# Kernel optimization log

Hardware: AMD Instinct MI355X
Metric: run time of the kernel (lower is better)

## Reference

```python
import jax, jax.numpy as jnp
import numpy as np

EPS = 1e-5  # torch BatchNorm2d default


def _conv(x, w, padding):
    return jax.lax.conv_general_dilated(
        x, w, window_strides=(1, 1),
        padding=[(padding, padding), (padding, padding)],
        dimension_numbers=("NCHW", "OIHW", "NCHW"))


def _bn(x, gamma, beta):
    # training-mode batchnorm (biased variance), matching nn.BatchNorm2d forward
    mu = x.mean(axis=(0, 2, 3), keepdims=True)
    var = x.var(axis=(0, 2, 3), keepdims=True)
    xn = (x - mu) * jax.lax.rsqrt(var + EPS)
    return gamma[None, :, None, None] * xn + beta[None, :, None, None]


def _ste(x):
    # forward: sign(x); backward: pass gradient where |x| <= 1 (STE)
    m = (jnp.abs(x) <= 1.0).astype(x.dtype)
    s = jax.lax.stop_gradient(jnp.sign(x))
    return s + m * x - jax.lax.stop_gradient(m * x)


def _binconv(x, w, alpha, padding=1):
    # XNOR-style: sign both operands, full-precision conv, scale by alpha
    return _conv(jnp.sign(x), jnp.sign(w), padding) * alpha


def _maxpool2(x):
    return jax.lax.reduce_window(x, -jnp.inf, jax.lax.max,
                                 (1, 1, 2, 2), (1, 1, 2, 2), "VALID")


def setup_inputs() -> dict:
    key = jax.random.key(0)
    ks = jax.random.split(key, 8)

    def kaiming(k, shape):
        fan_out = shape[0] * shape[2] * shape[3]
        std = np.sqrt(2.0 / fan_out)
        return jax.random.normal(k, shape, dtype=jnp.float32) * std

    return {
        "x": jax.random.normal(ks[0], (128, 1, 128, 128), dtype=jnp.float32),
        # first conv (full precision) 1->32, k=3, pad=1
        "w1": kaiming(ks[1], (32, 1, 3, 3)),
        "b1": jnp.zeros((32,), jnp.float32),
        "g1": jnp.ones((32,), jnp.float32),
        "beta1": jnp.zeros((32,), jnp.float32),
        # BinaryConv2d 32->32
        "w2": kaiming(ks[2], (32, 32, 3, 3)),
        "a2": jnp.ones((1,), jnp.float32),
        "g2": jnp.ones((32,), jnp.float32),
        "beta2": jnp.zeros((32,), jnp.float32),
        # BinaryConv2d 32->64
        "w3": kaiming(ks[3], (64, 32, 3, 3)),
        "a3": jnp.ones((1,), jnp.float32),
        "g3": jnp.ones((64,), jnp.float32),
        "beta3": jnp.zeros((64,), jnp.float32),
        # BinaryConv2d 64->128
        "w4": kaiming(ks[4], (128, 64, 3, 3)),
        "a4": jnp.ones((1,), jnp.float32),
        # classifier 128->10
        "wf": jax.random.normal(ks[5], (10, 128), dtype=jnp.float32) * (1.0 / np.sqrt(128.0)),
        "bf": jnp.zeros((10,), jnp.float32),
    }


def reference(x, w1, b1, g1, beta1, w2, a2, g2, beta2, w3, a3, g3, beta3, w4, a4, wf, bf):
    h = _conv(x, w1, padding=1) + b1[None, :, None, None]   # [N,32,128,128]
    h = _bn(h, g1, beta1)
    h = _ste(h)
    h = _binconv(h, w2, a2)                                 # [N,32,128,128]
    h = _maxpool2(h)                                        # [N,32,64,64]
    h = _bn(h, g2, beta2)
    h = _ste(h)
    h = _binconv(h, w3, a3)                                 # [N,64,64,64]
    h = _maxpool2(h)                                        # [N,64,32,32]
    h = _bn(h, g3, beta3)
    h = _ste(h)
    h = _binconv(h, w4, a4)                                 # [N,128,32,32]
    h = h.mean(axis=(2, 3))                                 # AdaptiveAvgPool2d(1) -> [N,128]
    return h @ wf.T + bf                                    # [N,10]
```

## Files before the change

kernel.cpp:

```cpp
#include <hip/hip_runtime.h>
#include <stdint.h>

constexpr int NB = 128;

__global__ void pack_weights_all_kernel(const float* __restrict__ w2, const float* __restrict__ w3,
                                        const float* __restrict__ w4,
                                        uint32_t* __restrict__ wp2, uint32_t* __restrict__ wp3,
                                        uint32_t* __restrict__ wp4)
{
    int idx = blockIdx.x * blockDim.x + threadIdx.x;
    const float* w; uint32_t* o; int ICW, i;
    if (idx < 288)       { w = w2; o = wp2; ICW = 1; i = idx; }
    else if (idx < 864)  { w = w3; o = wp3; ICW = 1; i = idx - 288; }
    else if (idx < 3168) { w = w4; o = wp4; ICW = 2; i = idx - 864; }
    else return;
    int iw = i % ICW;
    int t  = (i / ICW) % 9;
    int oc = i / (9 * ICW);
    int IC = ICW * 32;
    uint32_t word = 0;
    for (int b = 0; b < 32; ++b) {
        float wv = w[(size_t)(oc * IC + (iw * 32 + b)) * 9 + t];
        word |= (wv > 0.f ? 1u : 0u) << b;
    }
    o[i] = word;
}

__global__ void zero4_kernel(uint4* __restrict__ p, int n4)
{
    int i = blockIdx.x * blockDim.x + threadIdx.x;
    int stride = gridDim.x * blockDim.x;
    uint4 z = {0u, 0u, 0u, 0u};
    for (; i < n4; i += stride) p[i] = z;
}

__device__ __forceinline__ void conv1_load9(const float* __restrict__ x, int p, float* xv)
{
    int n = p >> 14;
    int y = (p >> 7) & 127;
    int c = p & 127;
    const float* xn = x + (size_t)n * 16384;
    #pragma unroll
    for (int ky = 0; ky < 3; ++ky)
    #pragma unroll
    for (int kx = 0; kx < 3; ++kx) {
        int yy = y + ky - 1, cc = c + kx - 1;
        float v = 0.f;
        if (yy >= 0 && yy < 128 && cc >= 0 && cc < 128) v = xn[yy * 128 + cc];
        xv[ky * 3 + kx] = v;
    }
}

__global__ __launch_bounds__(256) void xcorr_kernel(const float* __restrict__ x,
                                                    float* __restrict__ partials)
{
    __shared__ float wbuf[4][64];
    int tid = threadIdx.x;
    float s[9], c[45];
    #pragma unroll
    for (int t = 0; t < 9; ++t) s[t] = 0.f;
    #pragma unroll
    for (int q = 0; q < 45; ++q) c[q] = 0.f;

    int base = blockIdx.x * 256 + tid;
    #pragma unroll 4
    for (int k = 0; k < 16; ++k) {
        float xv[9];
        conv1_load9(x, base + k * 131072, xv);
        #pragma unroll
        for (int t = 0; t < 9; ++t) {
            s[t] += xv[t];
            #pragma unroll
            for (int u = t; u < 9; ++u) {
                int q = t * (19 - t) / 2 + (u - t);
                c[q] = fmaf(xv[t], xv[u], c[q]);
            }
        }
    }
    #pragma unroll
    for (int t = 0; t < 9; ++t) {
        float a = s[t];
        #pragma unroll
        for (int off = 32; off >= 1; off >>= 1) a += __shfl_xor(a, off, 64);
        s[t] = a;
    }
    #pragma unroll
    for (int q = 0; q < 45; ++q) {
        float a = c[q];
        #pragma unroll
        for (int off = 32; off >= 1; off >>= 1) a += __shfl_xor(a, off, 64);
        c[q] = a;
    }
    int lane = tid & 63, wv = tid >> 6;
    if (lane == 0) {
        #pragma unroll
        for (int t = 0; t < 9; ++t) wbuf[wv][t] = s[t];
        #pragma unroll
        for (int q = 0; q < 45; ++q) wbuf[wv][9 + q] = c[q];
    }
    __syncthreads();
    if (tid < 54)
        partials[blockIdx.x * 64 + tid] =
            (wbuf[0][tid] + wbuf[1][tid]) + (wbuf[2][tid] + wbuf[3][tid]);
}

__global__ void compute_ss1_kernel(const double* __restrict__ dsums,
                                   const float* __restrict__ w1, const float* __restrict__ b1,
                                   const float* __restrict__ g1, const float* __restrict__ be1,
                                   float* __restrict__ ss)
{
    __shared__ double S[9], C[45];
    int tid = threadIdx.x;
    if (tid < 9) S[tid] = dsums[tid];
    else if (tid < 54) C[tid - 9] = dsums[tid];
    __syncthreads();
    if (tid >= 32) return;
    double b = (double)b1[tid];
    double w[9];
    #pragma unroll
    for (int t = 0; t < 9; ++t) w[t] = (double)w1[tid * 9 + t];
    double Sdot = 0.0, Q = 0.0;
    #pragma unroll
    for (int t = 0; t < 9; ++t) {
        Sdot += w[t] * S[t];
        #pragma unroll
        for (int u = t; u < 9; ++u) {
            int q = t * (19 - t) / 2 + (u - t);
            double term = w[t] * w[u] * C[q];
            Q += (u == t) ? term : 2.0 * term;
        }
    }
    const double N = 2097152.0;
    double mu  = Sdot / N + b;
    double ex2 = (Q + 2.0 * b * Sdot) / N + b * b;
    float var = (float)(ex2 - mu * mu);
    float A = g1[tid] * (1.f / sqrtf(var + 1e-5f));
    ss[tid] = A;
    ss[32 + tid] = be1[tid] - (float)mu * A;
}

template<int CH, int STRIDE>
__global__ __launch_bounds__(256) void reduce_partials_kernel(
    const float* __restrict__ partials, int nblk, double* __restrict__ dsums)
{
    __shared__ double wsum[4];
    int ch = blockIdx.x;
    int tid = threadIdx.x;
    double a = 0.0;
    for (int i = tid; i < nblk; i += 256)
        a += (double)partials[(size_t)i * STRIDE + ch];
    #pragma unroll
    for (int off = 32; off >= 1; off >>= 1)
        a += __shfl_xor(a, off, 64);
    if ((tid & 63) == 0) wsum[tid >> 6] = a;
    __syncthreads();
    if (tid == 0)
        dsums[ch] = (wsum[0] + wsum[1]) + (wsum[2] + wsum[3]);
}

__global__ __launch_bounds__(256) void conv1_pack2_kernel(
    const float* __restrict__ x, const float* __restrict__ w1, const float* __restrict__ b1,
    const float* __restrict__ ss, uint32_t* __restrict__ s1p)
{
    int p = blockIdx.x * 256 + threadIdx.x;
    float xv[9];
    conv1_load9(x, p, xv);
    int n = p >> 14, y = (p >> 7) & 127, c = p & 127;

    uint32_t word = 0;
    for (int oc = 0; oc < 32; ++oc) {
        float a = xv[0] * w1[oc * 9];
        #pragma unroll
        for (int t = 1; t < 9; ++t) a = fmaf(xv[t], w1[oc * 9 + t], a);
        float A = ss[oc];
        float Bc = fmaf(A, b1[oc], ss[32 + oc]);
        float v = fmaf(A, a, Bc);
        word |= (v > 0.f ? 1u : 0u) << oc;
    }
    s1p[(size_t)n * 16900 + (y + 1) * 130 + (c + 1)] = word;
}

template<int OC, int PW, int LPW, int MAINB>
__global__ __launch_bounds__(256) void binconv_mainfix_kernel(
    const uint32_t* __restrict__ sp_in, const uint32_t* __restrict__ wp,
    const float* __restrict__ alpha, uint32_t* __restrict__ m16)
{
    constexpr int PS = 2 * PW + 2;
    constexpr int TOTAL = NB * PW * PW;
    int tid = threadIdx.x;
    bool useMax = (alpha[0] >= 0.f);

    if ((int)blockIdx.x < MAINB) {
        int p = blockIdx.x * 256 + tid;
        int px = p & (PW - 1), py = (p >> LPW) & (PW - 1), n = p >> (2 * LPW);
        bool border = (px == 0) | (px == PW - 1) | (py == 0) | (py == PW - 1);
        const uint32_t* base = sp_in + (size_t)n * PS * PS + (2 * py) * PS + 2 * px;

        uint32_t xw[16];
        #pragma unroll
        for (int r = 0; r < 4; ++r) {
            uint2 a = *(const uint2*)(base + r * PS);
            uint2 b = *(const uint2*)(base + r * PS + 2);
            xw[r * 4 + 0] = a.x; xw[r * 4 + 1] = a.y;
            xw[r * 4 + 2] = b.x; xw[r * 4 + 3] = b.y;
        }

        uint32_t pend = 0;
        for (int oc = 0; oc < OC; ++oc) {
            int s0 = 0, s1 = 0, s2 = 0, s3 = 0;
            #pragma unroll
            for (int ky = 0; ky < 3; ++ky)
            #pragma unroll
            for (int kx = 0; kx < 3; ++kx) {
                uint32_t wt = wp[oc * 9 + ky * 3 + kx];
                s0 += __popc(xw[ky * 4 + kx]           ^ wt);
                s1 += __popc(xw[ky * 4 + kx + 1]       ^ wt);
                s2 += __popc(xw[(ky + 1) * 4 + kx]     ^ wt);
                s3 += __popc(xw[(ky + 1) * 4 + kx + 1] ^ wt);
            }
            int sm = useMax ? min(min(s0, s1), min(s2, s3))
                            : max(max(s0, s1), max(s2, s3));
            int m = 288 - 2 * sm;
            if ((oc & 1) == 0) pend = (uint32_t)(uint16_t)(short)m;
            else if (!border)
                m16[(size_t)(oc >> 1) * TOTAL + p] = pend | ((uint32_t)(uint16_t)(short)m << 16);
        }
    } else {
        constexpr int RING = 4 * PW - 4;
        int t = ((int)blockIdx.x - MAINB) * 256 + tid;
        if (t >= NB * RING) return;
        int n = t / RING, r = t % RING;
        int py, px;
        if (r < PW)              { py = 0;      px = r; }
        else if (r < 2 * PW)     { py = PW - 1; px = r - PW; }
        else if (r < 3 * PW - 2) { px = 0;      py = r - 2 * PW + 1; }
        else                     { px = PW - 1; py = r - (3 * PW - 2) + 1; }
        int p = n * PW * PW + py * PW + px;
        const uint32_t* base = sp_in + (size_t)n * PS * PS + (2 * py) * PS + 2 * px;

        uint32_t xw[16], wm[16];
        #pragma unroll
        for (int a = 0; a < 4; ++a) {
            int rr = 2 * py - 1 + a;
            bool rv = (rr >= 0) && (rr < 2 * PW);
            #pragma unroll
            for (int b = 0; b < 4; ++b) {
                int cc = 2 * px - 1 + b;
                bool v = rv && (cc >= 0) && (cc < 2 * PW);
                wm[a * 4 + b] = v ? 0xFFFFFFFFu : 0u;
                xw[a * 4 + b] = base[a * PS + b];
            }
        }
        int cnt[4];
        #pragma unroll
        for (int a2 = 0; a2 < 2; ++a2)
        #pragma unroll
        for (int b2 = 0; b2 < 2; ++b2) {
            int cc = 0;
            #pragma unroll
            for (int ky = 0; ky < 3; ++ky)
            #pragma unroll
            for (int kx = 0; kx < 3; ++kx)
                cc += (int)(wm[(a2 + ky) * 4 + (b2 + kx)] & 1u);
            cnt[a2 * 2 + b2] = cc * 32;
        }

        uint32_t pend = 0;
        for (int oc = 0; oc < OC; ++oc) {
            int v[4];
            #pragma unroll
            for (int a2 = 0; a2 < 2; ++a2)
            #pragma unroll
            for (int b2 = 0; b2 < 2; ++b2) {
                int pop = 0;
                #pragma unroll
                for (int ky = 0; ky < 3; ++ky)
                #pragma unroll
                for (int kx = 0; kx < 3; ++kx) {
                    int idx = (a2 + ky) * 4 + (b2 + kx);
                    pop += __popc((xw[idx] ^ wp[oc * 9 + ky * 3 + kx]) & wm[idx]);
                }
                v[a2 * 2 + b2] = cnt[a2 * 2 + b2] - 2 * pop;
            }
            int m = useMax ? max(max(v[0], v[1]), max(v[2], v[3]))
                           : min(min(v[0], v[1]), min(v[2], v[3]));
            if ((oc & 1) == 0) pend = (uint32_t)(uint16_t)(short)m;
            else m16[(size_t)(oc >> 1) * TOTAL + p] = pend | ((uint32_t)(uint16_t)(short)m << 16);
        }
    }
}

template<int PIXELS, int CHUNKS>
__global__ __launch_bounds__(256) void stats16_kernel(const uint32_t* __restrict__ m16,
                                                      double* __restrict__ pd)
{
    __shared__ int wb[4][4];
    int bid = blockIdx.x;
    int q = bid / CHUNKS, ch = bid % CHUNKS;
    const uint32_t* pl = m16 + (size_t)q * PIXELS + (size_t)ch * (PIXELS / CHUNKS);
    int tid = threadIdx.x;
    int s0 = 0, s1 = 0, q0 = 0, q1 = 0;
    #pragma unroll 4
    for (int j = 0; j < PIXELS / CHUNKS / 256; ++j) {
        uint32_t u = pl[tid + j * 256];
        int m0 = (int)(short)(u & 0xffffu);
        int m1 = (int)u >> 16;
        s0 += m0; s1 += m1;
        q0 += m0 * m0; q1 += m1 * m1;
    }
    #pragma unroll
    for (int off = 32; off >= 1; off >>= 1) {
        s0 += __shfl_xor(s0, off, 64); s1 += __shfl_xor(s1, off, 64);
        q0 += __shfl_xor(q0, off, 64); q1 += __shfl_xor(q1, off, 64);
    }
    int lane = tid & 63, w = tid >> 6;
    if (lane == 0) { wb[w][0] = s0; wb[w][1] = s1; wb[w][2] = q0; wb[w][3] = q1; }
    __syncthreads();
    if (tid < 4)
        pd[(size_t)bid * 4 + tid] =
            (double)((long long)wb[0][tid] + wb[1][tid] + wb[2][tid] + wb[3][tid]);
}

template<int OC, int CHUNKS>
__global__ void finalize16_kernel(const double* __restrict__ pd,
                                  const float* __restrict__ gamma, const float* __restrict__ beta,
                                  const float* __restrict__ alpha,
                                  float inv_n, float* __restrict__ ss)
{
    __shared__ double sums[2 * OC];
    int tid = threadIdx.x;
    if (tid < 2 * OC) {
        bool issq = tid >= OC;
        int c = issq ? tid - OC : tid;
        int q = c >> 1;
        int slot = (issq ? 2 : 0) + (c & 1);
        double a = 0.0;
        #pragma unroll 4
        for (int i = 0; i < CHUNKS; ++i)
            a += pd[(size_t)(q * CHUNKS + i) * 4 + slot];
        sums[tid] = a;
    }
    __syncthreads();
    if (tid < OC) {
        double al = (double)alpha[0];
        float mu  = (float)(sums[tid] * al * (double)inv_n);
        float ex2 = (float)(sums[OC + tid] * al * al * (double)inv_n);
        float var = ex2 - mu * mu;
        float A = gamma[tid] * (1.f / sqrtf(var + 1e-5f));
        ss[tid] = A;
        ss[OC + tid] = beta[tid] - mu * A;
    }
}

template<int OC, int PW, int LPW, bool PADOUT>
__global__ __launch_bounds__(256) void binconv_pack_kernel(
    const uint32_t* __restrict__ m16, const float* __restrict__ alpha,
    const float* __restrict__ ss, void* __restrict__ sout)
{
    constexpr int TOTAL = NB * PW * PW;
    __shared__ float Ap[OC], Bp[OC];
    int tid = threadIdx.x;
    if (tid < OC) { Ap[tid] = ss[tid] * alpha[0]; Bp[tid] = ss[OC + tid]; }
    __syncthreads();
    int p = blockIdx.x * 256 + tid;
    uint64_t word = 0;
    #pragma unroll
    for (int q = 0; q < OC / 2; ++q) {
        uint32_t u = m16[(size_t)q * TOTAL + p];
        int m0 = (int)(short)(u & 0xffffu);
        int m1 = (int)u >> 16;
        float v0 = fmaf(Ap[2 * q],     (float)m0, Bp[2 * q]);
        float v1 = fmaf(Ap[2 * q + 1], (float)m1, Bp[2 * q + 1]);
        word |= (v0 > 0.f ? 1ull : 0ull) << (2 * q);
        word |= (v1 > 0.f ? 1ull : 0ull) << (2 * q + 1);
    }
    if constexpr (PADOUT) {
        int px = p & (PW - 1), py = (p >> LPW) & (PW - 1), n = p >> (2 * LPW);
        ((uint32_t*)sout)[(size_t)n * (PW + 2) * (PW + 2) + (py + 1) * (PW + 2) + (px + 1)]
            = (uint32_t)word;
    } else {
        ((uint64_t*)sout)[p] = word;
    }
}

__global__ __launch_bounds__(256) void conv4_partial_kernel(
    const uint64_t* __restrict__ s3, const uint64_t* __restrict__ wp4,
    float* __restrict__ p4)
{
    __shared__ uint64_t xt[192];
    __shared__ uint64_t wl[1152];
    __shared__ float red[256];
    int b = blockIdx.x;
    int n = b >> 3, s = b & 7;
    int tid = threadIdx.x;
    for (int i = tid; i < 192; i += 256) {
        int row = 4 * s - 1 + (i >> 5);
        int col = i & 31;
        xt[i] = (row >= 0 && row < 32) ? s3[(size_t)n * 1024 + row * 32 + col] : 0ull;
    }
    for (int i = tid; i < 1152; i += 256) wl[i] = wp4[i];
    __syncthreads();
    int oc = tid & 127, h = tid >> 7;
    uint64_t wr[9];
    #pragma unroll
    for (int t = 0; t < 9; ++t) wr[t] = wl[oc * 9 + t];
    int acc = 0;
    #pragma unroll
    for (int ry = 0; ry < 2; ++ry) {
        int lry = 2 * h + ry;
        int y = 4 * s + lry;
        for (int x = 0; x < 32; ++x) {
            int pop = 0, c = 0;
            #pragma unroll
            for (int ky = 0; ky < 3; ++ky) {
                int yy = y + ky - 1;
                if (yy < 0 || yy >= 32) continue;
                int lrow = lry + ky;
                #pragma unroll
                for (int kx = 0; kx < 3; ++kx) {
                    int xx = x + kx - 1;
                    if (xx < 0 || xx >= 32) continue;
                    pop += __popcll(xt[lrow * 32 + xx] ^ wr[ky * 3 + kx]);
                    c += 64;
                }
            }
            acc += c - 2 * pop;
        }
    }
    red[tid] = (float)acc;
    __syncthreads();
    if (tid < 128)
        p4[(size_t)b * 128 + tid] = red[tid] + red[tid + 128];
}

__global__ __launch_bounds__(128) void mean_linear_kernel(
    const float* __restrict__ p4, const float* __restrict__ alpha4,
    const float* __restrict__ wf, const float* __restrict__ bf, float* __restrict__ out)
{
    __shared__ float ml[128];
    int n = blockIdx.x, tid = threadIdx.x;
    float a = 0.f;
    #pragma unroll
    for (int s = 0; s < 8; ++s)
        a += p4[(size_t)((n * 8 + s) * 128) + tid];
    ml[tid] = a * alpha4[0] * (1.f / 1024.f);
    __syncthreads();
    if (tid < 10) {
        const float* w = wf + tid * 128;
        float acc = bf[tid];
        #pragma unroll 4
        for (int i = 0; i < 128; ++i) acc = fmaf(ml[i], w[i], acc);
        out[n * 10 + tid] = acc;
    }
}

extern "C" void kernel_launch(void* const* d_in, const int* in_sizes, int n_in,
                              void* d_out, int out_size, void* d_ws, size_t ws_size,
                              hipStream_t stream)
{
    const float* x   = (const float*)d_in[0];
    const float* w1  = (const float*)d_in[1];
    const float* b1  = (const float*)d_in[2];
    const float* g1  = (const float*)d_in[3];
    const float* be1 = (const float*)d_in[4];
    const float* w2  = (const float*)d_in[5];
    const float* a2  = (const float*)d_in[6];
    const float* g2  = (const float*)d_in[7];
    const float* be2 = (const float*)d_in[8];
    const float* w3  = (const float*)d_in[9];
    const float* a3  = (const float*)d_in[10];
    const float* g3  = (const float*)d_in[11];
    const float* be3 = (const float*)d_in[12];
    const float* w4  = (const float*)d_in[13];
    const float* a4  = (const float*)d_in[14];
    const float* wf  = (const float*)d_in[15];
    const float* bf  = (const float*)d_in[16];
    float* out = (float*)d_out;

    uint8_t* ws = (uint8_t*)d_ws;
    size_t off = 0;
    auto alloc = [&](size_t bytes) -> void* {
        void* p = ws + off;
        off += (bytes + 255) & ~(size_t)255;
        return p;
    };
    uint32_t* wp2 = (uint32_t*)alloc(288 * 4);
    uint32_t* wp3 = (uint32_t*)alloc(576 * 4);
    uint32_t* wp4 = (uint32_t*)alloc(2304 * 4);
    float* ss1 = (float*)alloc(64 * 4);
    float* ss2 = (float*)alloc(64 * 4);
    float* ss3 = (float*)alloc(128 * 4);
    double* dsums = (double*)alloc(256 * 8);
    double* pd    = (double*)alloc(2048 * 8);
    float* partials = (float*)alloc((size_t)512 * 64 * 4);
    uint32_t* s1p = (uint32_t*)alloc((size_t)128 * 16900 * 4);
    uint32_t* s2p = (uint32_t*)alloc((size_t)128 * 4356 * 4);
    uint64_t* s3  = (uint64_t*)alloc((size_t)128 * 1024 * 8);
    float* p4    = (float*)alloc((size_t)1024 * 128 * 4);
    uint32_t* m16_2 = (uint32_t*)alloc((size_t)16 * 524288 * 4);
    uint32_t* m16_3 = (uint32_t*)alloc((size_t)32 * 131072 * 4);

    {
        size_t span_bytes = (size_t)((uint8_t*)(s2p + (size_t)128 * 4356) - (uint8_t*)s1p);
        int n4 = (int)(span_bytes / 16);
        zero4_kernel<<<1024, 256, 0, stream>>>((uint4*)s1p, n4);
    }

    pack_weights_all_kernel<<<13, 256, 0, stream>>>(w2, w3, w4, wp2, wp3, wp4);

    xcorr_kernel<<<512, 256, 0, stream>>>(x, partials);
    reduce_partials_kernel<54, 64><<<54, 256, 0, stream>>>(partials, 512, dsums);
    compute_ss1_kernel<<<1, 64, 0, stream>>>(dsums, w1, b1, g1, be1, ss1);
    conv1_pack2_kernel<<<8192, 256, 0, stream>>>(x, w1, b1, ss1, s1p);

    binconv_mainfix_kernel<32, 64, 6, 2048><<<2048 + 126, 256, 0, stream>>>(s1p, wp2, a2, m16_2);
    stats16_kernel<524288, 32><<<512, 256, 0, stream>>>(m16_2, pd);
    finalize16_kernel<32, 32><<<1, 256, 0, stream>>>(pd, g2, be2, a2, 1.f / 524288.f, ss2);
    binconv_pack_kernel<32, 64, 6, true><<<2048, 256, 0, stream>>>(m16_2, a2, ss2, (void*)s2p);

    binconv_mainfix_kernel<64, 32, 5, 512><<<512 + 62, 256, 0, stream>>>(s2p, wp3, a3, m16_3);
    stats16_kernel<131072, 8><<<256, 256, 0, stream>>>(m16_3, pd);
    finalize16_kernel<64, 8><<<1, 256, 0, stream>>>(pd, g3, be3, a3, 1.f / 131072.f, ss3);
    binconv_pack_kernel<64, 32, 5, false><<<512, 256, 0, stream>>>(m16_3, a3, ss3, (void*)s3);

    conv4_partial_kernel<<<1024, 256, 0, stream>>>(s3, (const uint64_t*)wp4, p4);
    mean_linear_kernel<<<128, 128, 0, stream>>>(p4, a4, wf, bf, out);
}
```

Measured before the change: 222.0 us.

## Quad-tile binconv, fuse stats finalize, zero only borders, merge ss1 reduction

Several changes at once. Only the padding borders are zeroed instead of the whole buffers. The partial reduction is merged with the ss1 computation, and the conv1 weights are prefolded with the BN scale and shift. The binary conv now computes a 2x2 block of pooled outputs per thread, with weights staged in LDS, so inputs are reused across neighbouring outputs. The stats finalize step is folded into the stats kernel using a last-block atomic counter. Together these aim to cut launch count and redundant memory traffic, at the cost of higher register pressure and fewer blocks in the conv kernels.

After: 298.6 us. 34.5% more time.

```diff
diff --git a/kernel.cpp b/kernel.cpp
--- a/kernel.cpp
+++ b/kernel.cpp
@@ -26,12 +26,30 @@
     o[i] = word;
 }
 
-__global__ void zero4_kernel(uint4* __restrict__ p, int n4)
-{
-    int i = blockIdx.x * blockDim.x + threadIdx.x;
-    int stride = gridDim.x * blockDim.x;
-    uint4 z = {0u, 0u, 0u, 0u};
-    for (; i < n4; i += stride) p[i] = z;
+__global__ void zero_borders_kernel(uint32_t* __restrict__ s1p, uint32_t* __restrict__ s2p,
+                                    uint32_t* __restrict__ counters)
+{
+    int t = blockIdx.x * 256 + threadIdx.x;
+    if (t < 4) counters[t] = 0u;
+    const int total1 = 128 * 516;
+    if (t < total1) {
+        int n = t / 516, i = t % 516;
+        int r, c;
+        if (i < 130)      { r = 0;   c = i; }
+        else if (i < 260) { r = 129; c = i - 130; }
+        else { int j = i - 260; r = 1 + (j >> 1); c = (j & 1) ? 129 : 0; }
+        s1p[(size_t)n * 16900 + r * 130 + c] = 0u;
+    }
+    int t2 = t - total1;
+    const int total2 = 128 * 260;
+    if (t2 >= 0 && t2 < total2) {
+        int n = t2 / 260, i = t2 % 260;
+        int r, c;
+        if (i < 66)       { r = 0;  c = i; }
+        else if (i < 132) { r = 65; c = i - 66; }
+        else { int j = i - 132; r = 1 + (j >> 1); c = (j & 1) ? 65 : 0; }
+        s2p[(size_t)n * 4356 + r * 66 + c] = 0u;
+    }
 }
 
 __device__ __forceinline__ void conv1_load9(const float* __restrict__ x, int p, float* xv)
@@ -104,15 +122,35 @@
             (wbuf[0][tid] + wbuf[1][tid]) + (wbuf[2][tid] + wbuf[3][tid]);
 }
 
-__global__ void compute_ss1_kernel(const double* __restrict__ dsums,
-                                   const float* __restrict__ w1, const float* __restrict__ b1,
-                                   const float* __restrict__ g1, const float* __restrict__ be1,
-                                   float* __restrict__ ss)
-{
+__global__ __launch_bounds__(512) void reduce_ss1_kernel(
+    const float* __restrict__ partials, const float* __restrict__ w1, const float* __restrict__ b1,
+    const float* __restrict__ g1, const float* __restrict__ be1,
+    float* __restrict__ ss, float* __restrict__ w1f)
+{
+    __shared__ double red[54][8];
     __shared__ double S[9], C[45];
     int tid = threadIdx.x;
-    if (tid < 9) S[tid] = dsums[tid];
-    else if (tid < 54) C[tid - 9] = dsums[tid];
+    int ch = tid >> 3, part = tid & 7;
+    if (ch < 54) {
+        double a0 = 0.0, a1 = 0.0, a2 = 0.0, a3 = 0.0;
+        #pragma unroll 4
+        for (int j = 0; j < 64; ++j) {
+            double v = (double)partials[(size_t)(part + 8 * j) * 64 + ch];
+            if ((j & 3) == 0) a0 += v;
+            else if ((j & 3) == 1) a1 += v;
+            else if ((j & 3) == 2) a2 += v;
+            else a3 += v;
+        }
+        red[ch][part] = (a0 + a1) + (a2 + a3);
+    }
+    __syncthreads();
+    if (tid < 54) {
+        double a = 0.0;
+        #pragma unroll
+        for (int i = 0; i < 8; ++i) a += red[tid][i];
+        if (tid < 9) S[tid] = a;
+        else C[tid - 9] = a;
+    }
     __syncthreads();
     if (tid >= 32) return;
     double b = (double)b1[tid];
@@ -137,30 +175,15 @@
     float A = g1[tid] * (1.f / sqrtf(var + 1e-5f));
     ss[tid] = A;
     ss[32 + tid] = be1[tid] - (float)mu * A;
-}
-
-template<int CH, int STRIDE>
-__global__ __launch_bounds__(256) void reduce_partials_kernel(
-    const float* __restrict__ partials, int nblk, double* __restrict__ dsums)
-{
-    __shared__ double wsum[4];
-    int ch = blockIdx.x;
-    int tid = threadIdx.x;
-    double a = 0.0;
-    for (int i = tid; i < nblk; i += 256)
-        a += (double)partials[(size_t)i * STRIDE + ch];
-    #pragma unroll
-    for (int off = 32; off >= 1; off >>= 1)
-        a += __shfl_xor(a, off, 64);
-    if ((tid & 63) == 0) wsum[tid >> 6] = a;
-    __syncthreads();
-    if (tid == 0)
-        dsums[ch] = (wsum[0] + wsum[1]) + (wsum[2] + wsum[3]);
-}
-
-__global__ __launch_bounds__(256) void conv1_pack2_kernel(
-    const float* __restrict__ x, const float* __restrict__ w1, const float* __restrict__ b1,
-    const float* __restrict__ ss, uint32_t* __restrict__ s1p)
+    #pragma unroll
+    for (int t = 0; t < 9; ++t) w1f[tid * 12 + t] = w1[tid * 9 + t];
+    w1f[tid * 12 + 9]  = A;
+    w1f[tid * 12 + 10] = fmaf(A, b1[tid], be1[tid] - (float)mu * A);
+    w1f[tid * 12 + 11] = 0.f;
+}
+
+__global__ __launch_bounds__(256) void conv1_pack3_kernel(
+    const float* __restrict__ x, const float* __restrict__ w1f, uint32_t* __restrict__ s1p)
 {
     int p = blockIdx.x * 256 + threadIdx.x;
     float xv[9];
@@ -168,62 +191,108 @@
     int n = p >> 14, y = (p >> 7) & 127, c = p & 127;
 
     uint32_t word = 0;
+    #pragma unroll 4
     for (int oc = 0; oc < 32; ++oc) {
-        float a = xv[0] * w1[oc * 9];
-        #pragma unroll
-        for (int t = 1; t < 9; ++t) a = fmaf(xv[t], w1[oc * 9 + t], a);
-        float A = ss[oc];
-        float Bc = fmaf(A, b1[oc], ss[32 + oc]);
-        float v = fmaf(A, a, Bc);
+        const float* wf = w1f + oc * 12;
+        float a = xv[0] * wf[0];
+        a = fmaf(xv[1], wf[1], a);
+        a = fmaf(xv[2], wf[2], a);
+        a = fmaf(xv[3], wf[3], a);
+        a = fmaf(xv[4], wf[4], a);
+        a = fmaf(xv[5], wf[5], a);
+        a = fmaf(xv[6], wf[6], a);
+        a = fmaf(xv[7], wf[7], a);
+        a = fmaf(xv[8], wf[8], a);
+        float v = fmaf(wf[9], a, wf[10]);
         word |= (v > 0.f ? 1u : 0u) << oc;
     }
     s1p[(size_t)n * 16900 + (y + 1) * 130 + (c + 1)] = word;
 }
 
-template<int OC, int PW, int LPW, int MAINB>
-__global__ __launch_bounds__(256) void binconv_mainfix_kernel(
+template<int OC, int PW, int LQW, int MAINB>
+__global__ __launch_bounds__(256) void binconv_quad_kernel(
     const uint32_t* __restrict__ sp_in, const uint32_t* __restrict__ wp,
     const float* __restrict__ alpha, uint32_t* __restrict__ m16)
 {
     constexpr int PS = 2 * PW + 2;
+    constexpr int QW = PW / 2;
     constexpr int TOTAL = NB * PW * PW;
+    __shared__ uint32_t wl[OC * 12];
     int tid = threadIdx.x;
+    for (int i = tid; i < OC * 9; i += 256) wl[(i / 9) * 12 + (i % 9)] = wp[i];
+    __syncthreads();
     bool useMax = (alpha[0] >= 0.f);
 
     if ((int)blockIdx.x < MAINB) {
         int p = blockIdx.x * 256 + tid;
-        int px = p & (PW - 1), py = (p >> LPW) & (PW - 1), n = p >> (2 * LPW);
-        bool border = (px == 0) | (px == PW - 1) | (py == 0) | (py == PW - 1);
-        const uint32_t* base = sp_in + (size_t)n * PS * PS + (2 * py) * PS + 2 * px;
-
-        uint32_t xw[16];
-        #pragma unroll
-        for (int r = 0; r < 4; ++r) {
-            uint2 a = *(const uint2*)(base + r * PS);
-            uint2 b = *(const uint2*)(base + r * PS + 2);
-            xw[r * 4 + 0] = a.x; xw[r * 4 + 1] = a.y;
-            xw[r * 4 + 2] = b.x; xw[r * 4 + 3] = b.y;
-        }
-
-        uint32_t pend = 0;
+        int qx = p & (QW - 1), qy = (p >> LQW) & (QW - 1), n = p >> (2 * LQW);
+        const uint32_t* base = sp_in + (size_t)n * PS * PS + (4 * qy) * PS + 4 * qx;
+
+        uint32_t xw[36];
+        #pragma unroll
+        for (int r = 0; r < 6; ++r) {
+            uint4 a = *(const uint4*)(base + r * PS);
+            uint2 b = *(const uint2*)(base + r * PS + 4);
+            xw[r * 6 + 0] = a.x; xw[r * 6 + 1] = a.y; xw[r * 6 + 2] = a.z;
+            xw[r * 6 + 3] = a.w; xw[r * 6 + 4] = b.x; xw[r * 6 + 5] = b.y;
+        }
+
+        bool okT = (qy != 0), okB = (qy != QW - 1);
+        bool okL = (qx != 0), okR = (qx != QW - 1);
+        int rowbase = (n * PW + 2 * qy) * PW + 2 * qx;
+
+        uint32_t mprev[4];
         for (int oc = 0; oc < OC; ++oc) {
-            int s0 = 0, s1 = 0, s2 = 0, s3 = 0;
+            uint4 wa = *(const uint4*)&wl[oc * 12];
+            uint4 wb = *(const uint4*)&wl[oc * 12 + 4];
+            uint32_t w8 = wl[oc * 12 + 8];
+            uint32_t w[9] = {wa.x, wa.y, wa.z, wa.w, wb.x, wb.y, wb.z, wb.w, w8};
+
+            int s[16];
+            #pragma unroll
+            for (int i = 0; i < 16; ++i) s[i] = 0;
             #pragma unroll
             for (int ky = 0; ky < 3; ++ky)
             #pragma unroll
             for (int kx = 0; kx < 3; ++kx) {
-                uint32_t wt = wp[oc * 9 + ky * 3 + kx];
-                s0 += __popc(xw[ky * 4 + kx]           ^ wt);
-                s1 += __popc(xw[ky * 4 + kx + 1]       ^ wt);
-                s2 += __popc(xw[(ky + 1) * 4 + kx]     ^ wt);
-                s3 += __popc(xw[(ky + 1) * 4 + kx + 1] ^ wt);
-            }
-            int sm = useMax ? min(min(s0, s1), min(s2, s3))
-                            : max(max(s0, s1), max(s2, s3));
-            int m = 288 - 2 * sm;
-            if ((oc & 1) == 0) pend = (uint32_t)(uint16_t)(short)m;
-            else if (!border)
-                m16[(size_t)(oc >> 1) * TOTAL + p] = pend | ((uint32_t)(uint16_t)(short)m << 16);
+                uint32_t wt = w[ky * 3 + kx];
+                #pragma unroll
+                for (int r0 = 0; r0 < 4; ++r0)
+                #pragma unroll
+                for (int c0 = 0; c0 < 4; ++c0)
+                    s[r0 * 4 + c0] += __popc(xw[(r0 + ky) * 6 + (c0 + kx)] ^ wt);
+            }
+
+            uint32_t mcur[4];
+            #pragma unroll
+            for (int iy = 0; iy < 2; ++iy)
+            #pragma unroll
+            for (int ix = 0; ix < 2; ++ix) {
+                int a  = s[(2 * iy) * 4 + 2 * ix],     b2 = s[(2 * iy) * 4 + 2 * ix + 1];
+                int cc = s[(2 * iy + 1) * 4 + 2 * ix], d  = s[(2 * iy + 1) * 4 + 2 * ix + 1];
+                int sm = useMax ? min(min(a, b2), min(cc, d)) : max(max(a, b2), max(cc, d));
+                mcur[iy * 2 + ix] = (uint32_t)(uint16_t)(short)(288 - 2 * sm);
+            }
+
+            if (oc & 1) {
+                size_t pbase = (size_t)(oc >> 1) * TOTAL + rowbase;
+                #pragma unroll
+                for (int iy = 0; iy < 2; ++iy) {
+                    bool okY = iy ? okB : okT;
+                    if (!okY) continue;
+                    uint32_t v0 = mprev[iy * 2]     | (mcur[iy * 2]     << 16);
+                    uint32_t v1 = mprev[iy * 2 + 1] | (mcur[iy * 2 + 1] << 16);
+                    size_t addr = pbase + (size_t)iy * PW;
+                    if (okL & okR) *(uint2*)&m16[addr] = make_uint2(v0, v1);
+                    else {
+                        if (okL) m16[addr] = v0;
+                        if (okR) m16[addr + 1] = v1;
+                    }
+                }
+            } else {
+                #pragma unroll
+                for (int i = 0; i < 4; ++i) mprev[i] = mcur[i];
+            }
         }
     } else {
         constexpr int RING = 4 * PW - 4;
@@ -267,6 +336,10 @@
 
         uint32_t pend = 0;
         for (int oc = 0; oc < OC; ++oc) {
+            uint4 wa = *(const uint4*)&wl[oc * 12];
+            uint4 wb = *(const uint4*)&wl[oc * 12 + 4];
+            uint32_t w8 = wl[oc * 12 + 8];
+            uint32_t w[9] = {wa.x, wa.y, wa.z, wa.w, wb.x, wb.y, wb.z, wb.w, w8};
             int v[4];
             #pragma unroll
             for (int a2 = 0; a2 < 2; ++a2)
@@ -278,7 +351,7 @@
                 #pragma unroll
                 for (int kx = 0; kx < 3; ++kx) {
                     int idx = (a2 + ky) * 4 + (b2 + kx);
-                    pop += __popc((xw[idx] ^ wp[oc * 9 + ky * 3 + kx]) & wm[idx]);
+                    pop += __popc((xw[idx] ^ w[ky * 3 + kx]) & wm[idx]);
                 }
                 v[a2 * 2 + b2] = cnt[a2 * 2 + b2] - 2 * pop;
             }
@@ -290,9 +363,11 @@
     }
 }
 
-template<int PIXELS, int CHUNKS>
-__global__ __launch_bounds__(256) void stats16_kernel(const uint32_t* __restrict__ m16,
-                                                      double* __restrict__ pd)
+template<int PIXELS, int CHUNKS, int OC>
+__global__ __launch_bounds__(256) void stats16_fin_kernel(
+    const uint32_t* __restrict__ m16, double* __restrict__ pd, uint32_t* __restrict__ counter,
+    const float* __restrict__ gamma, const float* __restrict__ beta,
+    const float* __restrict__ alpha, float inv_n, float* __restrict__ ss)
 {
     __shared__ int wb[4][4];
     int bid = blockIdx.x;
@@ -319,25 +394,25 @@
     if (tid < 4)
         pd[(size_t)bid * 4 + tid] =
             (double)((long long)wb[0][tid] + wb[1][tid] + wb[2][tid] + wb[3][tid]);
-}
-
-template<int OC, int CHUNKS>
-__global__ void finalize16_kernel(const double* __restrict__ pd,
-                                  const float* __restrict__ gamma, const float* __restrict__ beta,
-                                  const float* __restrict__ alpha,
-                                  float inv_n, float* __restrict__ ss)
-{
+
+    __threadfence();
+    __shared__ int lastflag;
+    if (tid == 0) lastflag = (atomicAdd(counter, 1u) == (uint32_t)(gridDim.x - 1)) ? 1 : 0;
+    __syncthreads();
+    if (!lastflag) return;
+    __threadfence();
+    if (tid == 0) *counter = 0u;
+
     __shared__ double sums[2 * OC];
-    int tid = threadIdx.x;
     if (tid < 2 * OC) {
         bool issq = tid >= OC;
         int c = issq ? tid - OC : tid;
-        int q = c >> 1;
+        int qq = c >> 1;
         int slot = (issq ? 2 : 0) + (c & 1);
         double a = 0.0;
         #pragma unroll 4
         for (int i = 0; i < CHUNKS; ++i)
-            a += pd[(size_t)(q * CHUNKS + i) * 4 + slot];
+            a += pd[(size_t)(qq * CHUNKS + i) * 4 + slot];
         sums[tid] = a;
     }
     __syncthreads();
@@ -490,7 +565,8 @@
     float* ss1 = (float*)alloc(64 * 4);
     float* ss2 = (float*)alloc(64 * 4);
     float* ss3 = (float*)alloc(128 * 4);
-    double* dsums = (double*)alloc(256 * 8);
+    float* w1f = (float*)alloc(384 * 4);
+    uint32_t* counters = (uint32_t*)alloc(4 * 4);
     double* pd    = (double*)alloc(2048 * 8);
     float* partials = (float*)alloc((size_t)512 * 64 * 4);
     uint32_t* s1p = (uint32_t*)alloc((size_t)128 * 16900 * 4);
@@ -500,27 +576,22 @@
     uint32_t* m16_2 = (uint32_t*)alloc((size_t)16 * 524288 * 4);
     uint32_t* m16_3 = (uint32_t*)alloc((size_t)32 * 131072 * 4);
 
-    {
-        size_t span_bytes = (size_t)((uint8_t*)(s2p + (size_t)128 * 4356) - (uint8_t*)s1p);
-        int n4 = (int)(span_bytes / 16);
-        zero4_kernel<<<1024, 256, 0, stream>>>((uint4*)s1p, n4);
-    }
+    zero_borders_kernel<<<388, 256, 0, stream>>>(s1p, s2p, counters);
 
     pack_weights_all_kernel<<<13, 256, 0, stream>>>(w2, w3, w4, wp2, wp3, wp4);
 
     xcorr_kernel<<<512, 256, 0, stream>>>(x, partials);
-    reduce_partials_kernel<54, 64><<<54, 256, 0, stream>>>(partials, 512, dsums);
-    compute_ss1_kernel<<<1, 64, 0, stream>>>(dsums, w1, b1, g1, be1, ss1);
-    conv1_pack2_kernel<<<8192, 256, 0, stream>>>(x, w1, b1, ss1, s1p);
-
-    binconv_mainfix_kernel<32, 64, 6, 2048><<<2048 + 126, 256, 0, stream>>>(s1p, wp2, a2, m16_2);
-    stats16_kernel<524288, 32><<<512, 256, 0, stream>>>(m16_2, pd);
-    finalize16_kernel<32, 32><<<1, 256, 0, stream>>>(pd, g2, be2, a2, 1.f / 524288.f, ss2);
+    reduce_ss1_kernel<<<1, 512, 0, stream>>>(partials, w1, b1, g1, be1, ss1, w1f);
+    conv1_pack3_kernel<<<8192, 256, 0, stream>>>(x, w1f, s1p);
+
+    binconv_quad_kernel<32, 64, 5, 512><<<512 + 126, 256, 0, stream>>>(s1p, wp2, a2, m16_2);
+    stats16_fin_kernel<524288, 32, 32><<<512, 256, 0, stream>>>(m16_2, pd, counters + 0,
+                                                                g2, be2, a2, 1.f / 524288.f, ss2);
     binconv_pack_kernel<32, 64, 6, true><<<2048, 256, 0, stream>>>(m16_2, a2, ss2, (void*)s2p);
 
-    binconv_mainfix_kernel<64, 32, 5, 512><<<512 + 62, 256, 0, stream>>>(s2p, wp3, a3, m16_3);
-    stats16_kernel<131072, 8><<<256, 256, 0, stream>>>(m16_3, pd);
-    finalize16_kernel<64, 8><<<1, 256, 0, stream>>>(pd, g3, be3, a3, 1.f / 131072.f, ss3);
+    binconv_quad_kernel<64, 32, 4, 128><<<128 + 62, 256, 0, stream>>>(s2p, wp3, a3, m16_3);
+    stats16_fin_kernel<131072, 8, 64><<<256, 256, 0, stream>>>(m16_3, pd, counters + 1,
+                                                               g3, be3, a3, 1.f / 131072.f, ss3);
     binconv_pack_kernel<64, 32, 5, false><<<512, 256, 0, stream>>>(m16_3, a3, ss3, (void*)s3);
 
     conv4_partial_kernel<<<1024, 256, 0, stream>>>(s3, (const uint64_t*)wp4, p4);
```
